# Kernel tuning notes

Measured on AMD Instinct MI355X. Metric: run time of the kernel, lower is better.

The kernel has to match this reference:

```python
import jax, jax.numpy as jnp
import numpy as np

N = 131072          # batch_size(64) * cycle_size(2048) total graph nodes
E = 2097152         # N * avg_degree(16) edges


def _gcn_block(x, edge_index, W_self, W_nbr, b):
    """GraphConv-style STGCN spatial block: self-transform + mean-aggregated
    neighbor transform over edge_index (gather -> segment-reduce -> scatter)."""
    src, dst = edge_index[0], edge_index[1]
    msg = jax.ops.segment_sum(x[src], dst, num_segments=N)            # [N, C_in]
    deg = jax.ops.segment_sum(jnp.ones((edge_index.shape[1],), x.dtype), dst,
                              num_segments=N)                          # [N]
    agg = msg / jnp.maximum(deg, 1.0)[:, None]
    return x @ W_self + agg @ W_nbr + b


def setup_inputs() -> dict:
    key = jax.random.key(0)
    ks = jax.random.split(key, 16)

    def lin(k, fan_in, fan_out):
        return jax.random.normal(k, (fan_in, fan_out), jnp.float32) / np.sqrt(fan_in)

    x = jax.random.normal(ks[0], (N, 16), jnp.float32)
    edge_index = jax.random.randint(ks[1], (2, E), 0, N)
    batch = jnp.zeros((N,), jnp.int64) if jax.config.jax_enable_x64 else jnp.zeros((N,), jnp.int32)

    return {
        "x": x,
        "edge_index": edge_index,
        "batch": batch,
        "W_lin": lin(ks[2], 16, 16),
        "b_lin": jnp.zeros((16,), jnp.float32),
        # block3: 16 -> 32
        "Ws3": lin(ks[3], 16, 32), "Wn3": lin(ks[4], 16, 32), "b3": jnp.zeros((32,), jnp.float32),
        # block2: 32 -> 64
        "Ws2": lin(ks[5], 32, 64), "Wn2": lin(ks[6], 32, 64), "b2": jnp.zeros((64,), jnp.float32),
        # block1: 64 -> 128
        "Ws1": lin(ks[7], 64, 128), "Wn1": lin(ks[8], 64, 128), "b1": jnp.zeros((128,), jnp.float32),
    }


def reference(x, edge_index, batch, W_lin, b_lin,
              Ws3, Wn3, b3, Ws2, Wn2, b2, Ws1, Wn1, b1):
    h = x @ W_lin + b_lin                                   # Linear(16,16)
    h = jax.nn.relu(_gcn_block(h, edge_index, Ws3, Wn3, b3))   # 16 -> 32
    h = jax.nn.relu(_gcn_block(h, edge_index, Ws2, Wn2, b2))   # 32 -> 64
    h = jax.nn.sigmoid(_gcn_block(h, edge_index, Ws1, Wn1, b1))  # 64 -> 128
    return h
```

## Files before the change

### kernel.cpp

```cpp
#include <hip/hip_runtime.h>
#include <cmath>


typedef __attribute__((ext_vector_type(8))) _Float16 half8;

#define NBUCKET 512
#define BUCKET_SHIFT 8

__global__ __launch_bounds__(256) void bucket_hist_kernel(
    const int* __restrict__ dst, int* __restrict__ bcnt, int E, int EPB, int nblk) {
    __shared__ int lh[NBUCKET];
    for (int i = threadIdx.x; i < NBUCKET; i += 256) lh[i] = 0;
    __syncthreads();
    int base = blockIdx.x * EPB;
    int end  = min(base + EPB, E);
    for (int i = base + threadIdx.x; i < end; i += 256)
        atomicAdd(&lh[dst[i] >> BUCKET_SHIFT], 1);
    __syncthreads();
    for (int i = threadIdx.x; i < NBUCKET; i += 256)
        bcnt[i * nblk + blockIdx.x] = lh[i];
}

__global__ void scan1_kernel(const int* __restrict__ in, int* __restrict__ out,
                             int* __restrict__ bsum) {
    __shared__ int s[256];
    int i = blockIdx.x * 256 + threadIdx.x;
    int v = in[i];
    s[threadIdx.x] = v;
    __syncthreads();
    for (int off = 1; off < 256; off <<= 1) {
        int t = (threadIdx.x >= off) ? s[threadIdx.x - off] : 0;
        __syncthreads();
        s[threadIdx.x] += t;
        __syncthreads();
    }
    out[i] = s[threadIdx.x] - v;
    if (threadIdx.x == 255) bsum[blockIdx.x] = s[255];
}

__global__ void scan2_kernel(int* __restrict__ bsum, int NB) {
    extern __shared__ int s2[];
    int v = (threadIdx.x < NB) ? bsum[threadIdx.x] : 0;
    s2[threadIdx.x] = v;
    __syncthreads();
    for (int off = 1; off < NB; off <<= 1) {
        int t = (threadIdx.x >= off) ? s2[threadIdx.x - off] : 0;
        __syncthreads();
        s2[threadIdx.x] += t;
        __syncthreads();
    }
    if (threadIdx.x < NB) bsum[threadIdx.x] = s2[threadIdx.x] - v;
}

__global__ void scan3_kernel(int* __restrict__ out, const int* __restrict__ bsum) {
    int i = blockIdx.x * 256 + threadIdx.x;
    out[i] += bsum[blockIdx.x];
}

__global__ __launch_bounds__(256) void partition_kernel(
    const int* __restrict__ src, const int* __restrict__ dst,
    const int* __restrict__ bofs, int2* __restrict__ part,
    int E, int EPB, int nblk) {
    __shared__ int cur[NBUCKET];
    for (int i = threadIdx.x; i < NBUCKET; i += 256)
        cur[i] = bofs[i * nblk + blockIdx.x];
    __syncthreads();
    int base = blockIdx.x * EPB;
    int end  = min(base + EPB, E);
    for (int i = base + threadIdx.x; i < end; i += 256) {
        int d = dst[i];
        int p = atomicAdd(&cur[d >> BUCKET_SHIFT], 1);
        part[p] = make_int2(src[i], d);
    }
}

__global__ __launch_bounds__(256) void local_csr_kernel(
    const int* __restrict__ bofs, const int2* __restrict__ part,
    int* __restrict__ row_ptr, int* __restrict__ csr_src,
    int N, int E, int nblk) {
    __shared__ int cnt[256];
    __shared__ int offs[256];
    const int u      = blockIdx.x;
    const int node0  = u << BUCKET_SHIFT;
    const int bstart = bofs[(size_t)u * nblk];
    const int bend   = (u + 1 < gridDim.x) ? bofs[(size_t)(u + 1) * nblk] : E;

    cnt[threadIdx.x] = 0;
    __syncthreads();
    for (int i = bstart + threadIdx.x; i < bend; i += 256)
        atomicAdd(&cnt[part[i].y - node0], 1);
    __syncthreads();

    int v = cnt[threadIdx.x];
    offs[threadIdx.x] = v;
    __syncthreads();
    for (int off = 1; off < 256; off <<= 1) {
        int t = (threadIdx.x >= off) ? offs[threadIdx.x - off] : 0;
        __syncthreads();
        offs[threadIdx.x] += t;
        __syncthreads();
    }
    int excl = offs[threadIdx.x] - v;
    int rbase = bstart + excl;
    if (node0 + threadIdx.x < N) row_ptr[node0 + threadIdx.x] = rbase;
    if (u == 0 && threadIdx.x == 0) row_ptr[N] = E;
    __syncthreads();
    cnt[threadIdx.x] = rbase;
    __syncthreads();
    for (int i = bstart + threadIdx.x; i < bend; i += 256) {
        int2 e = part[i];
        int p = atomicAdd(&cnt[e.y - node0], 1);
        csr_src[p] = e.x;
    }
}

__global__ void lin16_kernel(const float* __restrict__ x, const float* __restrict__ W,
                             const float* __restrict__ b, _Float16* __restrict__ h, int N) {
    __shared__ float sW[256];
    __shared__ float sb[16];
    sW[threadIdx.x] = W[threadIdx.x];
    if (threadIdx.x < 16) sb[threadIdx.x] = b[threadIdx.x];
    __syncthreads();
    int n = blockIdx.x * blockDim.x + threadIdx.x;
    if (n >= N) return;
    const float4* xr = (const float4*)(x + (size_t)n * 16);
    float4 x0 = xr[0], x1 = xr[1], x2 = xr[2], x3 = xr[3];
    float xi[16] = {x0.x, x0.y, x0.z, x0.w, x1.x, x1.y, x1.z, x1.w,
                    x2.x, x2.y, x2.z, x2.w, x3.x, x3.y, x3.z, x3.w};
    float o[16];
#pragma unroll
    for (int j = 0; j < 16; j++) o[j] = sb[j];
#pragma unroll
    for (int k = 0; k < 16; k++) {
        float xv = xi[k];
#pragma unroll
        for (int j = 0; j < 16; j++) o[j] += xv * sW[k * 16 + j];
    }
    half8 h0v, h1v;
#pragma unroll
    for (int j = 0; j < 8; j++) { h0v[j] = (_Float16)o[j]; h1v[j] = (_Float16)o[j + 8]; }
    half8* hr = (half8*)(h + (size_t)n * 16);
    hr[0] = h0v;
    hr[1] = h1v;
}

template <int C>
__global__ void gather_kernel(const int* __restrict__ row_ptr, const int* __restrict__ csr_src,
                              const _Float16* __restrict__ h, _Float16* __restrict__ agg, int N) {
    constexpr int GP = C / 8;
    int t = blockIdx.x * blockDim.x + threadIdx.x;
    int total = N * GP;
    if (t >= total) return;
    int n = t / GP;
    int g = t - n * GP;
    const int beg = row_ptr[n];
    const int end = row_ptr[n + 1];
    const size_t goff = (size_t)g * 8;

    float a0[8], a1[8];
#pragma unroll
    for (int i = 0; i < 8; i++) { a0[i] = 0.f; a1[i] = 0.f; }

    int j = beg;
    for (; j + 4 <= end; j += 4) {
        int i0 = csr_src[j + 0], i1 = csr_src[j + 1], i2 = csr_src[j + 2], i3 = csr_src[j + 3];
        half8 v0 = *(const half8*)(h + (size_t)i0 * C + goff);
        half8 v1 = *(const half8*)(h + (size_t)i1 * C + goff);
        half8 v2 = *(const half8*)(h + (size_t)i2 * C + goff);
        half8 v3 = *(const half8*)(h + (size_t)i3 * C + goff);
#pragma unroll
        for (int i = 0; i < 8; i++) {
            a0[i] += (float)v0[i] + (float)v2[i];
            a1[i] += (float)v1[i] + (float)v3[i];
        }
    }
    for (; j < end; ++j) {
        int i0 = csr_src[j];
        half8 v0 = *(const half8*)(h + (size_t)i0 * C + goff);
#pragma unroll
        for (int i = 0; i < 8; i++) a0[i] += (float)v0[i];
    }

    float inv = 1.0f / fmaxf((float)(end - beg), 1.0f);
    half8 r;
#pragma unroll
    for (int i = 0; i < 8; i++) r[i] = (_Float16)((a0[i] + a1[i]) * inv);
    *(half8*)(agg + (size_t)n * C + goff) = r;
}

template <int CI, int NOUT, int TM, int TN, int ACT>
__global__ __launch_bounds__(256) void gemm_kernel(
    const _Float16* __restrict__ hbuf, const _Float16* __restrict__ abuf,
    const float* __restrict__ Ws, const float* __restrict__ Wn,
    const float* __restrict__ bias, float* __restrict__ out, int N)
{
    constexpr int K   = 2 * CI;
    constexpr int BK  = (CI < 32) ? CI : 32;
    constexpr int KQ8 = BK / 8;
    constexpr int TX  = NOUT / TN;
    constexpr int TY  = 256 / TX;
    constexpr int BM  = TY * TM;
    constexpr int LDA = BK + 8;
    __shared__ float As[BM][LDA];
    __shared__ float Bs[BK][NOUT];

    const int tid  = threadIdx.x;
    const int tx   = tid % TX;
    const int ty   = tid / TX;
    const int row0 = blockIdx.x * BM;
    const int j0   = tx * TN;

    float acc[TM][TN];
#pragma unroll
    for (int r = 0; r < TM; r++)
#pragma unroll
        for (int j = 0; j < TN; j++) acc[r][j] = 0.0f;

#pragma unroll 1
    for (int k0 = 0; k0 < K; k0 += BK) {
        const _Float16* Asrc;
        const float* Bsrc;
        int ks;
        if (k0 < CI) { Asrc = hbuf; Bsrc = Ws; ks = k0; }
        else         { Asrc = abuf; Bsrc = Wn; ks = k0 - CI; }

        for (int idx = tid; idx < BM * KQ8; idx += 256) {
            int m  = idx / KQ8;
            int kq = idx - m * KQ8;
            half8 v = *(const half8*)(Asrc + (size_t)(row0 + m) * CI + ks + kq * 8);
            float4 f0, f1;
            f0.x = (float)v[0]; f0.y = (float)v[1]; f0.z = (float)v[2]; f0.w = (float)v[3];
            f1.x = (float)v[4]; f1.y = (float)v[5]; f1.z = (float)v[6]; f1.w = (float)v[7];
            *(float4*)&As[m][kq * 8]     = f0;
            *(float4*)&As[m][kq * 8 + 4] = f1;
        }
        for (int idx = tid; idx < BK * (NOUT / 4); idx += 256) {
            int kk = idx / (NOUT / 4);
            int jq = idx - kk * (NOUT / 4);
            *(float4*)&Bs[kk][jq * 4] =
                *(const float4*)(Bsrc + (size_t)(ks + kk) * NOUT + jq * 4);
        }
        __syncthreads();

#pragma unroll 8
        for (int k = 0; k < BK; k++) {
            float4 bv = *(const float4*)&Bs[k][j0];
            float a[TM];
#pragma unroll
            for (int r = 0; r < TM; r++) a[r] = As[ty + TY * r][k];
#pragma unroll
            for (int r = 0; r < TM; r++) {
                acc[r][0] += a[r] * bv.x;
                acc[r][1] += a[r] * bv.y;
                acc[r][2] += a[r] * bv.z;
                acc[r][3] += a[r] * bv.w;
            }
        }
        __syncthreads();
    }

    float4 bb = *(const float4*)(bias + j0);
#pragma unroll
    for (int r = 0; r < TM; r++) {
        size_t nrow = (size_t)(row0 + ty + TY * r);
        float4 v;
        v.x = acc[r][0] + bb.x;
        v.y = acc[r][1] + bb.y;
        v.z = acc[r][2] + bb.z;
        v.w = acc[r][3] + bb.w;
        if (ACT == 0) {
            v.x = fmaxf(v.x, 0.0f); v.y = fmaxf(v.y, 0.0f);
            v.z = fmaxf(v.z, 0.0f); v.w = fmaxf(v.w, 0.0f);
        } else {
            v.x = 1.0f / (1.0f + __expf(-v.x));
            v.y = 1.0f / (1.0f + __expf(-v.y));
            v.z = 1.0f / (1.0f + __expf(-v.z));
            v.w = 1.0f / (1.0f + __expf(-v.w));
        }
        *(float4*)(out + nrow * NOUT + j0) = v;
    }
}

template <int CI, int NOUT, int TM, int TN, int ACT>
__global__ __launch_bounds__(256) void gemm_h_kernel(
    const _Float16* __restrict__ hbuf, const _Float16* __restrict__ abuf,
    const float* __restrict__ Ws, const float* __restrict__ Wn,
    const float* __restrict__ bias, _Float16* __restrict__ out, int N)
{
    constexpr int K   = 2 * CI;
    constexpr int BK  = (CI < 32) ? CI : 32;
    constexpr int KQ8 = BK / 8;
    constexpr int TX  = NOUT / TN;
    constexpr int TY  = 256 / TX;
    constexpr int BM  = TY * TM;
    constexpr int LDA = BK + 8;
    __shared__ float As[BM][LDA];
    __shared__ float Bs[BK][NOUT];

    const int tid  = threadIdx.x;
    const int tx   = tid % TX;
    const int ty   = tid / TX;
    const int row0 = blockIdx.x * BM;
    const int j0   = tx * TN;

    float acc[TM][TN];
#pragma unroll
    for (int r = 0; r < TM; r++)
#pragma unroll
        for (int j = 0; j < TN; j++) acc[r][j] = 0.0f;

#pragma unroll 1
    for (int k0 = 0; k0 < K; k0 += BK) {
        const _Float16* Asrc;
        const float* Bsrc;
        int ks;
        if (k0 < CI) { Asrc = hbuf; Bsrc = Ws; ks = k0; }
        else         { Asrc = abuf; Bsrc = Wn; ks = k0 - CI; }

        for (int idx = tid; idx < BM * KQ8; idx += 256) {
            int m  = idx / KQ8;
            int kq = idx - m * KQ8;
            half8 v = *(const half8*)(Asrc + (size_t)(row0 + m) * CI + ks + kq * 8);
            float4 f0, f1;
            f0.x = (float)v[0]; f0.y = (float)v[1]; f0.z = (float)v[2]; f0.w = (float)v[3];
            f1.x = (float)v[4]; f1.y = (float)v[5]; f1.z = (float)v[6]; f1.w = (float)v[7];
            *(float4*)&As[m][kq * 8]     = f0;
            *(float4*)&As[m][kq * 8 + 4] = f1;
        }
        for (int idx = tid; idx < BK * (NOUT / 4); idx += 256) {
            int kk = idx / (NOUT / 4);
            int jq = idx - kk * (NOUT / 4);
            *(float4*)&Bs[kk][jq * 4] =
                *(const float4*)(Bsrc + (size_t)(ks + kk) * NOUT + jq * 4);
        }
        __syncthreads();

#pragma unroll 8
        for (int k = 0; k < BK; k++) {
            float4 bv = *(const float4*)&Bs[k][j0];
            float a[TM];
#pragma unroll
            for (int r = 0; r < TM; r++) a[r] = As[ty + TY * r][k];
#pragma unroll
            for (int r = 0; r < TM; r++) {
                acc[r][0] += a[r] * bv.x;
                acc[r][1] += a[r] * bv.y;
                acc[r][2] += a[r] * bv.z;
                acc[r][3] += a[r] * bv.w;
            }
        }
        __syncthreads();
    }

    float4 bb = *(const float4*)(bias + j0);
#pragma unroll
    for (int r = 0; r < TM; r++) {
        size_t nrow = (size_t)(row0 + ty + TY * r);
        float v0 = acc[r][0] + bb.x;
        float v1 = acc[r][1] + bb.y;
        float v2 = acc[r][2] + bb.z;
        float v3 = acc[r][3] + bb.w;
        if (ACT == 0) {
            v0 = fmaxf(v0, 0.0f); v1 = fmaxf(v1, 0.0f);
            v2 = fmaxf(v2, 0.0f); v3 = fmaxf(v3, 0.0f);
        } else {
            v0 = 1.0f / (1.0f + __expf(-v0));
            v1 = 1.0f / (1.0f + __expf(-v1));
            v2 = 1.0f / (1.0f + __expf(-v2));
            v3 = 1.0f / (1.0f + __expf(-v3));
        }
        typedef __attribute__((ext_vector_type(4))) _Float16 half4;
        half4 hv;
        hv[0] = (_Float16)v0; hv[1] = (_Float16)v1;
        hv[2] = (_Float16)v2; hv[3] = (_Float16)v3;
        *(half4*)(out + nrow * NOUT + j0) = hv;
    }
}

extern "C" void kernel_launch(void* const* d_in, const int* in_sizes, int n_in,
                              void* d_out, int out_size, void* d_ws, size_t ws_size,
                              hipStream_t stream) {
    const float* x     = (const float*)d_in[0];
    const int*   ei    = (const int*)d_in[1];
    const float* W_lin = (const float*)d_in[3];
    const float* b_lin = (const float*)d_in[4];
    const float* Ws3   = (const float*)d_in[5];
    const float* Wn3   = (const float*)d_in[6];
    const float* b3    = (const float*)d_in[7];
    const float* Ws2   = (const float*)d_in[8];
    const float* Wn2   = (const float*)d_in[9];
    const float* b2    = (const float*)d_in[10];
    const float* Ws1   = (const float*)d_in[11];
    const float* Wn1   = (const float*)d_in[12];
    const float* b1    = (const float*)d_in[13];
    float* out = (float*)d_out;

    const int N = in_sizes[0] / 16;
    const int E = in_sizes[1] / 2;
    const int* src = ei;
    const int* dst = ei + E;

    const int NBLK = 512;
    const int EPB  = (E + NBLK - 1) / NBLK;
    const int M    = NBUCKET * NBLK;
    const int NB2  = M / 256;

    int* wsi = (int*)d_ws;
    int* row_ptr = wsi;
    size_t B0 = ((size_t)(N + 1) + 3) & ~(size_t)3;
    int* bcnt = wsi + B0;
    int* bofs = bcnt + M;
    int* bsum = bofs + M;
    size_t C0 = (B0 + 2 * (size_t)M + (size_t)NB2 + 3) & ~(size_t)3;
    int* csr_src = wsi + C0;
    size_t P0 = (C0 + (size_t)E + 3) & ~(size_t)3;
    int2* part = (int2*)(wsi + P0);
    size_t H0 = (P0 + 2 * (size_t)E + 3) & ~(size_t)3;
    _Float16* regA = (_Float16*)(wsi + H0);
    _Float16* regB = regA + (size_t)64 * N;

    _Float16* h0    = regA;
    _Float16* agg16 = regA + (size_t)16 * N;
    _Float16* h2    = regA;
    _Float16* h3    = regB;
    _Float16* agg32 = regB + (size_t)32 * N;
    _Float16* agg64 = regB;

    const int BLK = 256;

    bucket_hist_kernel<<<NBLK, 256, 0, stream>>>(dst, bcnt, E, EPB, NBLK);
    scan1_kernel<<<NB2, 256, 0, stream>>>(bcnt, bofs, bsum);
    scan2_kernel<<<1, NB2, NB2 * sizeof(int), stream>>>(bsum, NB2);
    scan3_kernel<<<NB2, 256, 0, stream>>>(bofs, bsum);
    partition_kernel<<<NBLK, 256, 0, stream>>>(src, dst, bofs, part, E, EPB, NBLK);
    local_csr_kernel<<<NBUCKET, 256, 0, stream>>>(bofs, part, row_ptr, csr_src, N, E, NBLK);

    lin16_kernel<<<(N + BLK - 1) / BLK, BLK, 0, stream>>>(x, W_lin, b_lin, h0, N);

    gather_kernel<16><<<((size_t)N * 2 + BLK - 1) / BLK, BLK, 0, stream>>>(row_ptr, csr_src, h0, agg16, N);
    gemm_h_kernel<16, 32, 4, 4, 0><<<N / 128, 256, 0, stream>>>(h0, agg16, Ws3, Wn3, b3, h3, N);

    gather_kernel<32><<<((size_t)N * 4 + BLK - 1) / BLK, BLK, 0, stream>>>(row_ptr, csr_src, h3, agg32, N);
    gemm_h_kernel<32, 64, 8, 4, 0><<<N / 128, 256, 0, stream>>>(h3, agg32, Ws2, Wn2, b2, h2, N);

    gather_kernel<64><<<((size_t)N * 8 + BLK - 1) / BLK, BLK, 0, stream>>>(row_ptr, csr_src, h2, agg64, N);
    gemm_kernel<64, 128, 8, 4, 1><<<N / 64, 256, 0, stream>>>(h2, agg64, Ws1, Wn1, b1, out, N);
}
```

Before: 377.4 us.

## Replace scalar FP32 GEMMs with MFMA f16 kernels using pre-transposed half weights

Adds a small kernel that converts and transposes the self and neighbor weight matrices into a single f16 [NOUT][2*CI] layout. The three dense transforms now use a kernel built on mfma_f32_16x16x32_f16, with A fragments read directly from global memory instead of scalar FMA tiles staged in shared memory. This removes the shared-memory staging of activations and FP32 conversion overhead. In exchange, weights are rounded to f16, and the output stores become per-element scalar writes that may coalesce less well.

```diff
diff --git a/kernel.cpp b/kernel.cpp
--- a/kernel.cpp
+++ b/kernel.cpp
@@ -3,6 +3,7 @@
 
 
 typedef __attribute__((ext_vector_type(8))) _Float16 half8;
+typedef __attribute__((ext_vector_type(4))) float floatx4;
 
 #define NBUCKET 512
 #define BUCKET_SHIFT 8
@@ -112,6 +113,16 @@
         int p = atomicAdd(&cnt[e.y - node0], 1);
         csr_src[p] = e.x;
     }
+}
+
+__global__ void wt_kernel(const float* __restrict__ Ws, const float* __restrict__ Wn,
+                          _Float16* __restrict__ Wt, int CI, int NOUT) {
+    int K = 2 * CI;
+    int idx = blockIdx.x * 256 + threadIdx.x;
+    if (idx >= NOUT * K) return;
+    int n = idx / K, k = idx - n * K;
+    float v = (k < CI) ? Ws[(size_t)k * NOUT + n] : Wn[(size_t)(k - CI) * NOUT + n];
+    Wt[idx] = (_Float16)v;
 }
 
 __global__ void lin16_kernel(const float* __restrict__ x, const float* __restrict__ W,
@@ -188,192 +199,63 @@
     *(half8*)(agg + (size_t)n * C + goff) = r;
 }
 
-template <int CI, int NOUT, int TM, int TN, int ACT>
-__global__ __launch_bounds__(256) void gemm_kernel(
+template <int CI, int NOUT, int ACT, bool OUT_F16>
+__global__ __launch_bounds__(256) void mfma_gemm_kernel(
     const _Float16* __restrict__ hbuf, const _Float16* __restrict__ abuf,
-    const float* __restrict__ Ws, const float* __restrict__ Wn,
-    const float* __restrict__ bias, float* __restrict__ out, int N)
+    const _Float16* __restrict__ Wt,
+    const float* __restrict__ bias, void* __restrict__ outp, int N)
 {
     constexpr int K   = 2 * CI;
-    constexpr int BK  = (CI < 32) ? CI : 32;
-    constexpr int KQ8 = BK / 8;
-    constexpr int TX  = NOUT / TN;
-    constexpr int TY  = 256 / TX;
-    constexpr int BM  = TY * TM;
-    constexpr int LDA = BK + 8;
-    __shared__ float As[BM][LDA];
-    __shared__ float Bs[BK][NOUT];
-
-    const int tid  = threadIdx.x;
-    const int tx   = tid % TX;
-    const int ty   = tid / TX;
-    const int row0 = blockIdx.x * BM;
-    const int j0   = tx * TN;
-
-    float acc[TM][TN];
-#pragma unroll
-    for (int r = 0; r < TM; r++)
-#pragma unroll
-        for (int j = 0; j < TN; j++) acc[r][j] = 0.0f;
-
-#pragma unroll 1
-    for (int k0 = 0; k0 < K; k0 += BK) {
-        const _Float16* Asrc;
-        const float* Bsrc;
-        int ks;
-        if (k0 < CI) { Asrc = hbuf; Bsrc = Ws; ks = k0; }
-        else         { Asrc = abuf; Bsrc = Wn; ks = k0 - CI; }
-
-        for (int idx = tid; idx < BM * KQ8; idx += 256) {
-            int m  = idx / KQ8;
-            int kq = idx - m * KQ8;
-            half8 v = *(const half8*)(Asrc + (size_t)(row0 + m) * CI + ks + kq * 8);
-            float4 f0, f1;
-            f0.x = (float)v[0]; f0.y = (float)v[1]; f0.z = (float)v[2]; f0.w = (float)v[3];
-            f1.x = (float)v[4]; f1.y = (float)v[5]; f1.z = (float)v[6]; f1.w = (float)v[7];
-            *(float4*)&As[m][kq * 8]     = f0;
-            *(float4*)&As[m][kq * 8 + 4] = f1;
+    constexpr int KS  = K / 32;
+    constexpr int CT  = NOUT / 16;
+    constexpr int LDW = K + 8;
+    __shared__ _Float16 Bt[NOUT * LDW];
+
+    const int tid = threadIdx.x;
+    for (int idx = tid; idx < NOUT * (K / 8); idx += 256) {
+        int n  = idx / (K / 8);
+        int kq = idx - n * (K / 8);
+        *(half8*)&Bt[n * LDW + kq * 8] = *(const half8*)(Wt + (size_t)n * K + kq * 8);
+    }
+    __syncthreads();
+
+    const int wave = tid >> 6;
+    const int lane = tid & 63;
+    const int m    = lane & 15;
+    const int quad = lane >> 4;
+    const int row0 = blockIdx.x * 64 + wave * 16;
+    const size_t row = (size_t)(row0 + m);
+
+    floatx4 acc[CT];
+#pragma unroll
+    for (int c = 0; c < CT; c++) acc[c] = (floatx4){0.f, 0.f, 0.f, 0.f};
+
+#pragma unroll
+    for (int s = 0; s < KS; s++) {
+        int k8 = s * 32 + quad * 8;
+        const _Float16* Ap = (k8 < CI) ? (hbuf + row * CI + k8)
+                                       : (abuf + row * CI + (k8 - CI));
+        half8 a = *(const half8*)Ap;
+#pragma unroll
+        for (int c = 0; c < CT; c++) {
+            half8 b = *(const half8*)&Bt[(c * 16 + m) * LDW + k8];
+            acc[c] = __builtin_amdgcn_mfma_f32_16x16x32_f16(a, b, acc[c], 0, 0, 0);
         }
-        for (int idx = tid; idx < BK * (NOUT / 4); idx += 256) {
-            int kk = idx / (NOUT / 4);
-            int jq = idx - kk * (NOUT / 4);
-            *(float4*)&Bs[kk][jq * 4] =
-                *(const float4*)(Bsrc + (size_t)(ks + kk) * NOUT + jq * 4);
+    }
+
+#pragma unroll
+    for (int c = 0; c < CT; c++) {
+        int col = c * 16 + m;
+        float bv = bias[col];
+#pragma unroll
+        for (int j = 0; j < 4; j++) {
+            int orow = row0 + quad * 4 + j;
+            float v = acc[c][j] + bv;
+            if (ACT == 0) v = fmaxf(v, 0.0f);
+            else          v = 1.0f / (1.0f + __expf(-v));
+            if (OUT_F16) ((_Float16*)outp)[(size_t)orow * NOUT + col] = (_Float16)v;
+            else         ((float*)outp)[(size_t)orow * NOUT + col] = v;
         }
-        __syncthreads();
-
-#pragma unroll 8
-        for (int k = 0; k < BK; k++) {
-            float4 bv = *(const float4*)&Bs[k][j0];
-            float a[TM];
-#pragma unroll
-            for (int r = 0; r < TM; r++) a[r] = As[ty + TY * r][k];
-#pragma unroll
-            for (int r = 0; r < TM; r++) {
-                acc[r][0] += a[r] * bv.x;
-                acc[r][1] += a[r] * bv.y;
-                acc[r][2] += a[r] * bv.z;
-                acc[r][3] += a[r] * bv.w;
-            }
-        }
-        __syncthreads();
-    }
-
-    float4 bb = *(const float4*)(bias + j0);
-#pragma unroll
-    for (int r = 0; r < TM; r++) {
-        size_t nrow = (size_t)(row0 + ty + TY * r);
-        float4 v;
-        v.x = acc[r][0] + bb.x;
-        v.y = acc[r][1] + bb.y;
-        v.z = acc[r][2] + bb.z;
-        v.w = acc[r][3] + bb.w;
-        if (ACT == 0) {
-            v.x = fmaxf(v.x, 0.0f); v.y = fmaxf(v.y, 0.0f);
-            v.z = fmaxf(v.z, 0.0f); v.w = fmaxf(v.w, 0.0f);
-        } else {
-            v.x = 1.0f / (1.0f + __expf(-v.x));
-            v.y = 1.0f / (1.0f + __expf(-v.y));
-            v.z = 1.0f / (1.0f + __expf(-v.z));
-            v.w = 1.0f / (1.0f + __expf(-v.w));
-        }
-        *(float4*)(out + nrow * NOUT + j0) = v;
-    }
-}
-
-template <int CI, int NOUT, int TM, int TN, int ACT>
-__global__ __launch_bounds__(256) void gemm_h_kernel(
-    const _Float16* __restrict__ hbuf, const _Float16* __restrict__ abuf,
-    const float* __restrict__ Ws, const float* __restrict__ Wn,
-    const float* __restrict__ bias, _Float16* __restrict__ out, int N)
-{
-    constexpr int K   = 2 * CI;
-    constexpr int BK  = (CI < 32) ? CI : 32;
-    constexpr int KQ8 = BK / 8;
-    constexpr int TX  = NOUT / TN;
-    constexpr int TY  = 256 / TX;
-    constexpr int BM  = TY * TM;
-    constexpr int LDA = BK + 8;
-    __shared__ float As[BM][LDA];
-    __shared__ float Bs[BK][NOUT];
-
-    const int tid  = threadIdx.x;
-    const int tx   = tid % TX;
-    const int ty   = tid / TX;
-    const int row0 = blockIdx.x * BM;
-    const int j0   = tx * TN;
-
-    float acc[TM][TN];
-#pragma unroll
-    for (int r = 0; r < TM; r++)
-#pragma unroll
-        for (int j = 0; j < TN; j++) acc[r][j] = 0.0f;
-
-#pragma unroll 1
-    for (int k0 = 0; k0 < K; k0 += BK) {
-        const _Float16* Asrc;
-        const float* Bsrc;
-        int ks;
-        if (k0 < CI) { Asrc = hbuf; Bsrc = Ws; ks = k0; }
-        else         { Asrc = abuf; Bsrc = Wn; ks = k0 - CI; }
-
-        for (int idx = tid; idx < BM * KQ8; idx += 256) {
-            int m  = idx / KQ8;
-            int kq = idx - m * KQ8;
-            half8 v = *(const half8*)(Asrc + (size_t)(row0 + m) * CI + ks + kq * 8);
-            float4 f0, f1;
-            f0.x = (float)v[0]; f0.y = (float)v[1]; f0.z = (float)v[2]; f0.w = (float)v[3];
-            f1.x = (float)v[4]; f1.y = (float)v[5]; f1.z = (float)v[6]; f1.w = (float)v[7];
-            *(float4*)&As[m][kq * 8]     = f0;
-            *(float4*)&As[m][kq * 8 + 4] = f1;
-        }
-        for (int idx = tid; idx < BK * (NOUT / 4); idx += 256) {
-            int kk = idx / (NOUT / 4);
-            int jq = idx - kk * (NOUT / 4);
-            *(float4*)&Bs[kk][jq * 4] =
-                *(const float4*)(Bsrc + (size_t)(ks + kk) * NOUT + jq * 4);
-        }
-        __syncthreads();
-
-#pragma unroll 8
-        for (int k = 0; k < BK; k++) {
-            float4 bv = *(const float4*)&Bs[k][j0];
-            float a[TM];
-#pragma unroll
-            for (int r = 0; r < TM; r++) a[r] = As[ty + TY * r][k];
-#pragma unroll
-            for (int r = 0; r < TM; r++) {
-                acc[r][0] += a[r] * bv.x;
-                acc[r][1] += a[r] * bv.y;
-                acc[r][2] += a[r] * bv.z;
-                acc[r][3] += a[r] * bv.w;
-            }
-        }
-        __syncthreads();
-    }
-
-    float4 bb = *(const float4*)(bias + j0);
-#pragma unroll
-    for (int r = 0; r < TM; r++) {
-        size_t nrow = (size_t)(row0 + ty + TY * r);
-        float v0 = acc[r][0] + bb.x;
-        float v1 = acc[r][1] + bb.y;
-        float v2 = acc[r][2] + bb.z;
-        float v3 = acc[r][3] + bb.w;
-        if (ACT == 0) {
-            v0 = fmaxf(v0, 0.0f); v1 = fmaxf(v1, 0.0f);
-            v2 = fmaxf(v2, 0.0f); v3 = fmaxf(v3, 0.0f);
-        } else {
-            v0 = 1.0f / (1.0f + __expf(-v0));
-            v1 = 1.0f / (1.0f + __expf(-v1));
-            v2 = 1.0f / (1.0f + __expf(-v2));
-            v3 = 1.0f / (1.0f + __expf(-v3));
-        }
-        typedef __attribute__((ext_vector_type(4))) _Float16 half4;
-        half4 hv;
-        hv[0] = (_Float16)v0; hv[1] = (_Float16)v1;
-        hv[2] = (_Float16)v2; hv[3] = (_Float16)v3;
-        *(half4*)(out + nrow * NOUT + j0) = hv;
     }
 }
 
@@ -418,6 +300,9 @@
     size_t H0 = (P0 + 2 * (size_t)E + 3) & ~(size_t)3;
     _Float16* regA = (_Float16*)(wsi + H0);
     _Float16* regB = regA + (size_t)64 * N;
+    _Float16* Wt1  = regB + (size_t)64 * N;
+    _Float16* Wt2  = Wt1 + 16384;
+    _Float16* Wt3  = Wt2 + 4096;
 
     _Float16* h0    = regA;
     _Float16* agg16 = regA + (size_t)16 * N;
@@ -428,6 +313,10 @@
 
     const int BLK = 256;
 
+    wt_kernel<<<(32 * 32 + 255) / 256, 256, 0, stream>>>(Ws3, Wn3, Wt3, 16, 32);
+    wt_kernel<<<(64 * 64 + 255) / 256, 256, 0, stream>>>(Ws2, Wn2, Wt2, 32, 64);
+    wt_kernel<<<(128 * 128 + 255) / 256, 256, 0, stream>>>(Ws1, Wn1, Wt1, 64, 128);
+
     bucket_hist_kernel<<<NBLK, 256, 0, stream>>>(dst, bcnt, E, EPB, NBLK);
     scan1_kernel<<<NB2, 256, 0, stream>>>(bcnt, bofs, bsum);
     scan2_kernel<<<1, NB2, NB2 * sizeof(int), stream>>>(bsum, NB2);
@@ -438,11 +327,11 @@
     lin16_kernel<<<(N + BLK - 1) / BLK, BLK, 0, stream>>>(x, W_lin, b_lin, h0, N);
 
     gather_kernel<16><<<((size_t)N * 2 + BLK - 1) / BLK, BLK, 0, stream>>>(row_ptr, csr_src, h0, agg16, N);
-    gemm_h_kernel<16, 32, 4, 4, 0><<<N / 128, 256, 0, stream>>>(h0, agg16, Ws3, Wn3, b3, h3, N);
+    mfma_gemm_kernel<16, 32, 0, true><<<N / 64, 256, 0, stream>>>(h0, agg16, Wt3, b3, h3, N);
 
     gather_kernel<32><<<((size_t)N * 4 + BLK - 1) / BLK, BLK, 0, stream>>>(row_ptr, csr_src, h3, agg32, N);
-    gemm_h_kernel<32, 64, 8, 4, 0><<<N / 128, 256, 0, stream>>>(h3, agg32, Ws2, Wn2, b2, h2, N);
+    mfma_gemm_kernel<32, 64, 0, true><<<N / 64, 256, 0, stream>>>(h3, agg32, Wt2, b2, h2, N);
 
     gather_kernel<64><<<((size_t)N * 8 + BLK - 1) / BLK, BLK, 0, stream>>>(row_ptr, csr_src, h2, agg64, N);
-    gemm_kernel<64, 128, 8, 4, 1><<<N / 64, 256, 0, stream>>>(h2, agg64, Ws1, Wn1, b1, out, N);
-}
+    mfma_gemm_kernel<64, 128, 1, false><<<N / 64, 256, 0, stream>>>(h2, agg64, Wt1, b1, out, N);
+}
```

Result: faster. 334.7 us (-11.3%).
